# Performance work log

Hardware: AMD Instinct MI355X
Metric: run time of the kernel (lower is better)

## Reference

```python
import jax, jax.numpy as jnp
from jax import lax
import numpy as np

B, T, E, H, DA, HEADS, V = 128, 512, 256, 256, 25, 5, 2080
NEG = -1e30


def setup_inputs() -> dict:
    key = jax.random.key(0)
    ks = jax.random.split(key, 10)
    word_ids = jax.random.randint(ks[0], (B, T), 0, V)
    lengths = jax.random.randint(ks[1], (B,), 1, T + 1)  # >=1, original skips empty captions
    emb = jax.random.normal(ks[2], (V, E), dtype=jnp.float32)  # normal_(0,1) init
    sc = 0.05
    W_ih_f = jax.random.normal(ks[3], (4 * H, E), dtype=jnp.float32) * sc
    W_hh_f = jax.random.normal(ks[4], (4 * H, H), dtype=jnp.float32) * sc
    W_ih_b = jax.random.normal(ks[5], (4 * H, E), dtype=jnp.float32) * sc
    W_hh_b = jax.random.normal(ks[6], (4 * H, H), dtype=jnp.float32) * sc
    b_f = jnp.zeros((4 * H,), jnp.float32)  # biases init constant 0
    b_b = jnp.zeros((4 * H,), jnp.float32)
    W_s1 = jax.random.normal(ks[7], (DA, 2 * H), dtype=jnp.float32) * sc
    W_s2 = jax.random.normal(ks[8], (HEADS, DA), dtype=jnp.float32) * sc
    return dict(word_ids=word_ids, lengths=lengths, emb=emb,
                W_ih_f=W_ih_f, W_hh_f=W_hh_f, b_f=b_f,
                W_ih_b=W_ih_b, W_hh_b=W_hh_b, b_b=b_b,
                W_s1=W_s1, W_s2=W_s2)


def _lstm(x, W_ih, W_hh, b):
    # x: [B,T,E] -> outputs [B,T,H]; PyTorch gate order i,f,g,o; zero init state
    px = jnp.einsum('bte,ge->tbg', x, W_ih) + b  # [T,B,4H], input proj precomputed
    h0 = jnp.zeros((x.shape[0], W_hh.shape[1]), x.dtype)

    def step(carry, p):
        h, c = carry
        g = p + h @ W_hh.T
        i, f, gg, o = jnp.split(g, 4, axis=-1)
        c = jax.nn.sigmoid(f) * c + jax.nn.sigmoid(i) * jnp.tanh(gg)
        h = jax.nn.sigmoid(o) * jnp.tanh(c)
        return (h, c), h

    _, hs = lax.scan(step, (h0, h0), px)
    return hs.transpose(1, 0, 2)  # [B,T,H]


def _forward(word_ids, lengths, emb, W_ih_f, W_hh_f, b_f, W_ih_b, W_hh_b, b_b, W_s1, W_s2):
    x = emb[word_ids]  # [B,T,E]
    tpos = jnp.arange(T)
    mask = tpos[None, :] < lengths[:, None]  # [B,T] valid positions
    # per-sample reversal within its own length (garbage tail comes after valid prefix)
    rev_idx = jnp.clip(lengths[:, None] - 1 - tpos[None, :], 0)  # [B,T]
    x_rev = jnp.take_along_axis(x, rev_idx[:, :, None], axis=1)
    h_fwd = _lstm(x, W_ih_f, W_hh_f, b_f)                       # [B,T,H]
    h_bwd_rev = _lstm(x_rev, W_ih_b, W_hh_b, b_b)
    h_bwd = jnp.take_along_axis(h_bwd_rev, rev_idx[:, :, None], axis=1)  # back to original order
    Hc = jnp.concatenate([h_fwd, h_bwd], axis=-1)               # [B,T,2H]
    # attention: softmax over time per head, masked to valid length
    s = jnp.tanh(Hc @ W_s1.T) @ W_s2.T                          # [B,T,heads]
    logits = jnp.where(mask[:, :, None], s, NEG)
    A = jax.nn.softmax(logits, axis=1).transpose(0, 2, 1)       # [B,heads,T]
    A = A * mask[:, None, :].astype(A.dtype)                    # exact zeros outside length
    M = jnp.einsum('bht,btd->bhd', A, Hc)                       # [B,heads,2H]
    sentence_embeddings = M.reshape(M.shape[0], -1)             # [B, heads*2H]
    AAt = jnp.einsum('bht,bgt->bhg', A, A)
    AAt = AAt * (1.0 - jnp.eye(HEADS, dtype=AAt.dtype))         # zero diagonal
    penal = jnp.sum(AAt * AAt) / M.shape[0]                     # mean of Frobenius^2
    return sentence_embeddings, penal


def reference(word_ids, lengths, emb, W_ih_f, W_hh_f, b_f, W_ih_b, W_hh_b, b_b, W_s1, W_s2):
    return _forward(word_ids, lengths, emb, W_ih_f, W_hh_f, b_f, W_ih_b, W_hh_b, b_b, W_s1, W_s2)
```

## Files before the change

### kernel.cpp

```cpp
#include <hip/hip_runtime.h>
#include <math.h>

#define T 512
#define B 128
#define E 256
#define H 256
#define G 1024
#define DA 25
#define HEADS 5
#define V 2080
#define NEGINF (-1e30f)

static constexpr size_t WBT_OFF  = 0;
static constexpr size_t WIH_OFF  = 1048576;
static constexpr size_t WS1M_OFF = 2097152;
static constexpr size_t PX_OFF   = 2148352;
static constexpr size_t HC_OFF   = 69257216;
static constexpr size_t HBUF_OFF = 203474944;
static constexpr size_t CST_OFF  = 203737088;
static constexpr size_t A_OFF    = 203999232;
static constexpr size_t PART_OFF = 205309952;
static constexpr size_t EMBH_OFF = 205310464;
static constexpr size_t EMBH_END = EMBH_OFF + (size_t)V * E * 2;

static constexpr unsigned LSTM_LDS_BYTES = 160304;

typedef _Float16 half2v __attribute__((ext_vector_type(2)));
typedef _Float16 half8_ __attribute__((ext_vector_type(8)));
typedef float    f32x4  __attribute__((ext_vector_type(4)));

__device__ __forceinline__ float sigmoidf_(float x) { return 1.f / (1.f + expf(-x)); }

__device__ __forceinline__ unsigned short f2h_(float f) {
    _Float16 h = (_Float16)f;
    unsigned short u;
    __builtin_memcpy(&u, &h, 2);
    return u;
}

__device__ __forceinline__ float fdot2_(unsigned w, half2v h, float acc) {
#if __has_builtin(__builtin_amdgcn_fdot2)
    half2v wv;
    __builtin_memcpy(&wv, &w, 4);
    return __builtin_amdgcn_fdot2(wv, h, acc, false);
#else
    unsigned short lo = (unsigned short)(w & 0xffffu), hi = (unsigned short)(w >> 16);
    _Float16 w0, w1;
    __builtin_memcpy(&w0, &lo, 2);
    __builtin_memcpy(&w1, &hi, 2);
    return fmaf((float)w0, (float)h[0], fmaf((float)w1, (float)h[1], acc));
#endif
}

__device__ __forceinline__ half2v packh2_(float a, float b) {
    half2v h;
    h[0] = (_Float16)a;
    h[1] = (_Float16)b;
    return h;
}

__global__ __launch_bounds__(256) void prep_kernel(const float* __restrict__ Whf,
                                                   const float* __restrict__ Whb,
                                                   const float* __restrict__ Wif,
                                                   const float* __restrict__ Wib,
                                                   const float* __restrict__ Ws1,
                                                   const float* __restrict__ emb,
                                                   unsigned short* __restrict__ wbt,
                                                   unsigned short* __restrict__ wih,
                                                   unsigned short* __restrict__ ws1m,
                                                   unsigned short* __restrict__ embh) {
    int idx = blockIdx.x * 256 + threadIdx.x;
    if (idx < 2 * G * H) {
        int d = idx >> 18;
        int rem = idx & 262143;
        int r = rem >> 8;
        int k = rem & 255;
        const float* W = d ? Whb : Whf;
        int gate = r >> 8, j = r & 255;
        int k2 = k >> 1, ke = k & 1;
        wbt[(((size_t)d * 128 + k2) * 256 + j) * 8 + gate * 2 + ke] = f2h_(W[(size_t)r * H + k]);
        const float* Wi = d ? Wib : Wif;
        wih[((size_t)d * G + r) * 256 + k] = f2h_(Wi[(size_t)r * E + k]);
    }
    if (idx < 32 * 512) {
        int r = idx >> 9, k = idx & 511;
        ws1m[idx] = (r < DA) ? f2h_(Ws1[r * 512 + k]) : (unsigned short)0;
    }
    if (embh && idx < V * E) embh[idx] = f2h_(emb[idx]);
}

__global__ __launch_bounds__(256) void proj_kernel(const int* __restrict__ word_ids,
                                                   const int* __restrict__ lengths,
                                                   const float* __restrict__ emb,
                                                   const unsigned* __restrict__ embh,
                                                   const unsigned* __restrict__ wih,
                                                   const float* __restrict__ bf,
                                                   const float* __restrict__ bb,
                                                   float* __restrict__ pxc, int chunk) {
    int g0 = blockIdx.x * 64;
    int b  = blockIdx.y;
    int d  = blockIdx.z;
    int len = lengths[b];
    int t0 = chunk * 64;
    if (t0 >= len) return;
    const float* bias = d ? bb : bf;

    __shared__ _Float16 A_s[64][264];
    __shared__ _Float16 B_s[64][264];

    int tid = threadIdx.x;
    int sr = tid >> 2, sq = tid & 3;

    {
        int t = t0 + sr;
        int src = d ? max(len - 1 - t, 0) : t;
        int wid = word_ids[b * T + src];
        if (embh) {
            const uint4* ap = (const uint4*)embh + (size_t)wid * 32;
            #pragma unroll
            for (int c = 0; c < 8; c++) {
                uint4 v = ap[sq * 8 + c];
                *(uint4*)&A_s[sr][(sq * 8 + c) * 8] = v;
            }
        } else {
            const float4* ep = (const float4*)(emb + (size_t)wid * E);
            #pragma unroll
            for (int c = 0; c < 8; c++) {
                float4 x0 = ep[(sq * 8 + c) * 2];
                float4 x1 = ep[(sq * 8 + c) * 2 + 1];
                half8_ hv;
                hv[0] = (_Float16)x0.x; hv[1] = (_Float16)x0.y;
                hv[2] = (_Float16)x0.z; hv[3] = (_Float16)x0.w;
                hv[4] = (_Float16)x1.x; hv[5] = (_Float16)x1.y;
                hv[6] = (_Float16)x1.z; hv[7] = (_Float16)x1.w;
                *(half8_*)&A_s[sr][(sq * 8 + c) * 8] = hv;
            }
        }
        const uint4* bp = (const uint4*)wih + ((size_t)d * G + g0 + sr) * 32;
        #pragma unroll
        for (int c = 0; c < 8; c++) {
            uint4 v = bp[sq * 8 + c];
            *(uint4*)&B_s[sr][(sq * 8 + c) * 8] = v;
        }
    }
    __syncthreads();

    int lane = tid & 63, wave = tid >> 6;
    int m0 = (wave >> 1) * 32;
    int n0 = (wave & 1) * 32;
    int lr = lane & 15, lq = lane >> 4;

    f32x4 acc00 = {0.f, 0.f, 0.f, 0.f}, acc01 = {0.f, 0.f, 0.f, 0.f};
    f32x4 acc10 = {0.f, 0.f, 0.f, 0.f}, acc11 = {0.f, 0.f, 0.f, 0.f};

    #pragma unroll
    for (int k0 = 0; k0 < E; k0 += 32) {
        int ka = k0 + lq * 8;
        half8_ af0 = *(const half8_*)&A_s[m0 + lr][ka];
        half8_ af1 = *(const half8_*)&A_s[m0 + 16 + lr][ka];
        half8_ bf0 = *(const half8_*)&B_s[n0 + lr][ka];
        half8_ bf1 = *(const half8_*)&B_s[n0 + 16 + lr][ka];
        acc00 = __builtin_amdgcn_mfma_f32_16x16x32_f16(af0, bf0, acc00, 0, 0, 0);
        acc01 = __builtin_amdgcn_mfma_f32_16x16x32_f16(af0, bf1, acc01, 0, 0, 0);
        acc10 = __builtin_amdgcn_mfma_f32_16x16x32_f16(af1, bf0, acc10, 0, 0, 0);
        acc11 = __builtin_amdgcn_mfma_f32_16x16x32_f16(af1, bf1, acc11, 0, 0, 0);
    }

    float bia0 = bias[g0 + n0 + lr];
    float bia1 = bias[g0 + n0 + 16 + lr];
    #pragma unroll
    for (int mi = 0; mi < 2; mi++) {
        f32x4 ar0 = mi ? acc10 : acc00;
        f32x4 ar1 = mi ? acc11 : acc01;
        #pragma unroll
        for (int rr = 0; rr < 4; rr++) {
            int s = m0 + mi * 16 + lq * 4 + rr;
            float* dst = pxc + ((size_t)(d * 64 + s) * B + b) * G + g0;
            dst[n0 + lr]      = ar0[rr] + bia0;
            dst[n0 + 16 + lr] = ar1[rr] + bia1;
        }
    }
}

__global__ __launch_bounds__(1024) void lstm6_kernel(const int* __restrict__ lengths,
                                                     const unsigned* __restrict__ wbt,
                                                     const float* __restrict__ pxc,
                                                     float* __restrict__ hc_out,
                                                     float* __restrict__ hbuf,
                                                     float* __restrict__ cstate,
                                                     int chunk) {
    int b   = blockIdx.x;
    int d   = blockIdx.y;
    int tid = threadIdx.x;
    int j  = tid & 255;
    int kq = tid >> 8;

    int len = lengths[b];
    int t0 = chunk * 64;
    if (t0 >= len) return;
    int tend = min(t0 + 64, len);

    extern __shared__ char smem[];
    unsigned* hh   = (unsigned*)smem;
    float4*   part = (float4*)(smem + 512);
    uint4*    wst  = (uint4*)(smem + 12848);

    float* hbufg = hbuf + ((size_t)d * B + b) * 256;

    float c = 0.f, hreg = 0.f;
    if (chunk == 0) {
        if (tid < 128) hh[tid] = 0u;
    } else {
        if (kq == 0) c = cstate[((size_t)d * B + b) * H + j];
        if (tid < 128) {
            half2v hv2 = packh2_(hbufg[2 * tid], hbufg[2 * tid + 1]);
            unsigned hu;
            __builtin_memcpy(&hu, &hv2, 4);
            hh[tid] = hu;
        }
    }

    const uint4* wp  = (const uint4*)wbt + ((size_t)d * 128 + kq * 32) * 256 + j;
    const float* pxd = pxc + (size_t)d * 64 * B * G;

    #pragma unroll
    for (int r = 0; r < 9; r++)
        wst[(kq * 9 + r) * 256 + j] = wp[(size_t)r * 256];
    uint4 wr0  = wp[9 * 256],  wr1  = wp[10 * 256], wr2  = wp[11 * 256];
    uint4 wr3  = wp[12 * 256], wr4  = wp[13 * 256], wr5  = wp[14 * 256];
    uint4 wr6  = wp[15 * 256], wr7  = wp[16 * 256], wr8  = wp[17 * 256];
    uint4 wr9  = wp[18 * 256], wr10 = wp[19 * 256], wr11 = wp[20 * 256];
    uint4 wr12 = wp[21 * 256], wr13 = wp[22 * 256], wr14 = wp[23 * 256];
    __syncthreads();

    int hlane = kq * 32 + (tid & 31);

    for (int t = t0; t < tend; t++) {
        int s = t - t0;
        float p0, p1, p2, p3;
        if (kq == 0) {
            const float* pxs = pxd + ((size_t)s * B + b) * G;
            p0 = pxs[j];
            p1 = pxs[256 + j];
            p2 = pxs[512 + j];
            p3 = pxs[768 + j];
        }
        float a0 = 0.f, a1 = 0.f, a2 = 0.f, a3 = 0.f;

        unsigned hlv = hh[hlane];

        #define HROW(IDX) __builtin_amdgcn_readlane(hlv, IDX)

        #pragma unroll
        for (int r = 24; r < 32; r++) {
            uint4 wv = wp[(size_t)r * 256];
            unsigned hu = HROW(r);
            half2v hhv;
            __builtin_memcpy(&hhv, &hu, 4);
            a0 = fdot2_(wv.x, hhv, a0);
            a1 = fdot2_(wv.y, hhv, a1);
            a2 = fdot2_(wv.z, hhv, a2);
            a3 = fdot2_(wv.w, hhv, a3);
        }
        #pragma unroll
        for (int r = 0; r < 9; r++) {
            uint4 wv = wst[(kq * 9 + r) * 256 + j];
            unsigned hu = HROW(r);
            half2v hhv;
            __builtin_memcpy(&hhv, &hu, 4);
            a0 = fdot2_(wv.x, hhv, a0);
            a1 = fdot2_(wv.y, hhv, a1);
            a2 = fdot2_(wv.z, hhv, a2);
            a3 = fdot2_(wv.w, hhv, a3);
        }
        {
            unsigned hu;
            half2v hv;
            #define RES_DOT(WR, IDX)                                   \
                hu = HROW(IDX);                                        \
                __builtin_memcpy(&hv, &hu, 4);                         \
                a0 = fdot2_(WR.x, hv, a0); a1 = fdot2_(WR.y, hv, a1);  \
                a2 = fdot2_(WR.z, hv, a2); a3 = fdot2_(WR.w, hv, a3);
            RES_DOT(wr0, 9)
            RES_DOT(wr1, 10)
            RES_DOT(wr2, 11)
            RES_DOT(wr3, 12)
            RES_DOT(wr4, 13)
            RES_DOT(wr5, 14)
            RES_DOT(wr6, 15)
            RES_DOT(wr7, 16)
            RES_DOT(wr8, 17)
            RES_DOT(wr9, 18)
            RES_DOT(wr10, 19)
            RES_DOT(wr11, 20)
            RES_DOT(wr12, 21)
            RES_DOT(wr13, 22)
            RES_DOT(wr14, 23)
            #undef RES_DOT
        }
        #undef HROW

        if (kq > 0) part[(kq - 1) * 257 + j] = make_float4(a0, a1, a2, a3);
        __syncthreads();

        if (kq == 0) {
            #pragma unroll
            for (int q = 0; q < 3; q++) {
                float4 qv = part[q * 257 + j];
                a0 += qv.x; a1 += qv.y; a2 += qv.z; a3 += qv.w;
            }
            a0 += p0; a1 += p1; a2 += p2; a3 += p3;

            float ig = sigmoidf_(a0), fg = sigmoidf_(a1), og = sigmoidf_(a3);
            c = fg * c + ig * tanhf(a2);
            float h = og * tanhf(c);
            hreg = h;

            float hn = __shfl_down(h, 1);
            if (!(j & 1)) {
                half2v hv2 = packh2_(h, hn);
                unsigned hu;
                __builtin_memcpy(&hu, &hv2, 4);
                hh[j >> 1] = hu;
            }
            int pos = d ? (len - 1 - t) : t;
            hc_out[((size_t)b * T + pos) * (2 * H) + d * H + j] = h;
        }
        __syncthreads();
    }

    if (kq == 0) {
        cstate[((size_t)d * B + b) * H + j] = c;
        hbufg[j] = hreg;
    }
}

__global__ __launch_bounds__(256) void logits_kernel(const int* __restrict__ lengths,
                                                     const float* __restrict__ hc,
                                                     const uint4* __restrict__ ws1m,
                                                     const float* __restrict__ Ws2,
                                                     float* __restrict__ S) {
    __shared__ _Float16 A_s[64][520];
    __shared__ _Float16 B_s[32][520];

    int b = blockIdx.y, tt = blockIdx.x;
    int tid = threadIdx.x;
    int len = lengths[b];
    int t0 = tt * 64;

    int lane = tid & 63, wave = tid >> 6;
    int lr = lane & 15, lq = lane >> 4;
    int m0 = wave * 16;

    if (t0 >= len) {
        if (lr < HEADS) {
            #pragma unroll
            for (int rr = 0; rr < 4; rr++) {
                int t = t0 + m0 + lq * 4 + rr;
                S[((size_t)b * HEADS + lr) * T + t] = NEGINF;
            }
        }
        return;
    }

    {
        #pragma unroll
        for (int i = 0; i < 8; i++) {
            int u = tid + i * 256;
            int r = u >> 6, c8 = u & 63;
            *(uint4*)&B_s[r][c8 * 8] = ws1m[u];
        }
    }
    {
        int row = tid >> 2, q = tid & 3;
        int t = t0 + row;
        const float4* ep = (const float4*)(hc + ((size_t)b * T + t) * 512 + q * 128);
        #pragma unroll
        for (int c = 0; c < 16; c++) {
            float4 x0 = ep[2 * c];
            float4 x1 = ep[2 * c + 1];
            half8_ hv;
            hv[0] = (_Float16)x0.x; hv[1] = (_Float16)x0.y;
            hv[2] = (_Float16)x0.z; hv[3] = (_Float16)x0.w;
            hv[4] = (_Float16)x1.x; hv[5] = (_Float16)x1.y;
            hv[6] = (_Float16)x1.z; hv[7] = (_Float16)x1.w;
            *(half8_*)&A_s[row][q * 128 + c * 8] = hv;
        }
    }
    __syncthreads();

    f32x4 acc0 = {0.f, 0.f, 0.f, 0.f};
    f32x4 acc1 = {0.f, 0.f, 0.f, 0.f};
    #pragma unroll
    for (int ks = 0; ks < 16; ks++) {
        int ka = ks * 32 + lq * 8;
        half8_ af  = *(const half8_*)&A_s[m0 + lr][ka];
        half8_ bf0 = *(const half8_*)&B_s[lr][ka];
        half8_ bf1 = *(const half8_*)&B_s[16 + lr][ka];
        acc0 = __builtin_amdgcn_mfma_f32_16x16x32_f16(af, bf0, acc0, 0, 0, 0);
        acc1 = __builtin_amdgcn_mfma_f32_16x16x32_f16(af, bf1, acc1, 0, 0, 0);
    }

    float w2a[HEADS], w2b[HEADS];
    #pragma unroll
    for (int h = 0; h < HEADS; h++) {
        w2a[h] = Ws2[h * DA + lr];
        w2b[h] = (lr + 16 < DA) ? Ws2[h * DA + 16 + lr] : 0.f;
    }

    #pragma unroll
    for (int rr = 0; rr < 4; rr++) {
        float y0 = tanhf(acc0[rr]);
        float y1 = tanhf(acc1[rr]);
        int t = t0 + m0 + lq * 4 + rr;
        float sv[HEADS];
        #pragma unroll
        for (int h = 0; h < HEADS; h++) {
            float v = y0 * w2a[h] + y1 * w2b[h];
            v += __shfl_xor(v, 1, 16);
            v += __shfl_xor(v, 2, 16);
            v += __shfl_xor(v, 4, 16);
            v += __shfl_xor(v, 8, 16);
            sv[h] = v;
        }
        if (lr < HEADS) {
            S[((size_t)b * HEADS + lr) * T + t] = (t < len) ? sv[lr] : NEGINF;
        }
    }
}

__global__ __launch_bounds__(256) void softmax_kernel(float* __restrict__ S) {
    int row = blockIdx.x;
    float* p = S + (size_t)row * T;
    int tid = threadIdx.x;
    int lane = tid & 63, wave = tid >> 6;
    __shared__ float rr[4], ss[4];

    float mx = NEGINF;
    #pragma unroll
    for (int i = 0; i < 2; i++) mx = fmaxf(mx, p[tid + i * 256]);
    for (int off = 32; off; off >>= 1) mx = fmaxf(mx, __shfl_xor(mx, off, 64));
    if (lane == 0) rr[wave] = mx;
    __syncthreads();
    mx = fmaxf(fmaxf(rr[0], rr[1]), fmaxf(rr[2], rr[3]));

    float e[2], sum = 0.f;
    #pragma unroll
    for (int i = 0; i < 2; i++) { e[i] = expf(p[tid + i * 256] - mx); sum += e[i]; }
    for (int off = 32; off; off >>= 1) sum += __shfl_xor(sum, off, 64);
    if (lane == 0) ss[wave] = sum;
    __syncthreads();
    sum = ss[0] + ss[1] + ss[2] + ss[3];
    float inv = 1.f / sum;
    #pragma unroll
    for (int i = 0; i < 2; i++) p[tid + i * 256] = e[i] * inv;
}

__global__ __launch_bounds__(256) void attnM_kernel(const int* __restrict__ lengths,
                                                    const float* __restrict__ A,
                                                    const float* __restrict__ hc,
                                                    float* __restrict__ out,
                                                    float* __restrict__ part) {
    int b = blockIdx.x, tid = threadIdx.x;
    int len = lengths[b];
    const float* Ab  = A + (size_t)b * HEADS * T;
    const float* hcb = hc + (size_t)b * T * (2 * H);
    float acc[HEADS][2];
    #pragma unroll
    for (int h = 0; h < HEADS; h++) { acc[h][0] = 0.f; acc[h][1] = 0.f; }
    float p[10];
    #pragma unroll
    for (int i = 0; i < 10; i++) p[i] = 0.f;

    for (int t = 0; t < len; t++) {
        float v0 = hcb[(size_t)t * (2 * H) + tid];
        float v1 = hcb[(size_t)t * (2 * H) + H + tid];
        float a0 = Ab[t], a1 = Ab[T + t], a2 = Ab[2 * T + t], a3 = Ab[3 * T + t], a4 = Ab[4 * T + t];
        acc[0][0] += a0 * v0; acc[0][1] += a0 * v1;
        acc[1][0] += a1 * v0; acc[1][1] += a1 * v1;
        acc[2][0] += a2 * v0; acc[2][1] += a2 * v1;
        acc[3][0] += a3 * v0; acc[3][1] += a3 * v1;
        acc[4][0] += a4 * v0; acc[4][1] += a4 * v1;
        if ((t & 255) == tid) {
            p[0] += a0 * a1; p[1] += a0 * a2; p[2] += a0 * a3; p[3] += a0 * a4;
            p[4] += a1 * a2; p[5] += a1 * a3; p[6] += a1 * a4;
            p[7] += a2 * a3; p[8] += a2 * a4; p[9] += a3 * a4;
        }
    }
    #pragma unroll
    for (int h = 0; h < HEADS; h++) {
        out[(size_t)b * (HEADS * 2 * H) + h * (2 * H) + tid]     = acc[h][0];
        out[(size_t)b * (HEADS * 2 * H) + h * (2 * H) + H + tid] = acc[h][1];
    }

    __shared__ float red[10][4];
    int lane = tid & 63, wave = tid >> 6;
    #pragma unroll
    for (int i = 0; i < 10; i++) {
        float v = p[i];
        for (int off = 32; off; off >>= 1) v += __shfl_xor(v, off, 64);
        if (lane == 0) red[i][wave] = v;
    }
    __syncthreads();
    if (tid == 0) {
        float s = 0.f;
        #pragma unroll
        for (int i = 0; i < 10; i++) {
            float P = red[i][0] + red[i][1] + red[i][2] + red[i][3];
            s += 2.f * P * P;
        }
        part[b] = s;
    }
}

__global__ __launch_bounds__(128) void final_kernel(const float* __restrict__ part,
                                                    float* __restrict__ out) {
    int tid = threadIdx.x;
    float v = part[tid];
    for (int off = 32; off; off >>= 1) v += __shfl_xor(v, off, 64);
    __shared__ float r2[2];
    if ((tid & 63) == 0) r2[tid >> 6] = v;
    __syncthreads();
    if (tid == 0) out[(size_t)B * HEADS * 2 * H] = (r2[0] + r2[1]) * (1.f / (float)B);
}

extern "C" void kernel_launch(void* const* d_in, const int* in_sizes, int n_in,
                              void* d_out, int out_size, void* d_ws, size_t ws_size,
                              hipStream_t stream) {
    const int*   word_ids = (const int*)d_in[0];
    const int*   lengths  = (const int*)d_in[1];
    const float* emb      = (const float*)d_in[2];
    const float* W_ih_f   = (const float*)d_in[3];
    const float* W_hh_f   = (const float*)d_in[4];
    const float* b_f      = (const float*)d_in[5];
    const float* W_ih_b   = (const float*)d_in[6];
    const float* W_hh_b   = (const float*)d_in[7];
    const float* b_b      = (const float*)d_in[8];
    const float* W_s1     = (const float*)d_in[9];
    const float* W_s2     = (const float*)d_in[10];
    float* out = (float*)d_out;

    char* ws = (char*)d_ws;
    unsigned short* wbt16 = (unsigned short*)(ws + WBT_OFF);
    unsigned*       wbt   = (unsigned*)(ws + WBT_OFF);
    unsigned short* wih16 = (unsigned short*)(ws + WIH_OFF);
    unsigned*       wihu  = (unsigned*)(ws + WIH_OFF);
    unsigned short* ws1m16 = (unsigned short*)(ws + WS1M_OFF);
    const uint4*    ws1m4  = (const uint4*)(ws + WS1M_OFF);
    float* pxc    = (float*)(ws + PX_OFF);
    float* hc     = (float*)(ws + HC_OFF);
    float* hbuf   = (float*)(ws + HBUF_OFF);
    float* cstate = (float*)(ws + CST_OFF);
    float* Abuf   = (float*)(ws + A_OFF);
    float* part   = (float*)(ws + PART_OFF);
    bool have_embh = (ws_size >= EMBH_END);
    unsigned short* embh16 = have_embh ? (unsigned short*)(ws + EMBH_OFF) : nullptr;
    const unsigned* embhu  = have_embh ? (const unsigned*)(ws + EMBH_OFF) : nullptr;

    prep_kernel<<<2080, 256, 0, stream>>>(W_hh_f, W_hh_b, W_ih_f, W_ih_b, W_s1, emb,
                                          wbt16, wih16, ws1m16, embh16);

    for (int c = 0; c < 8; c++) {
        proj_kernel<<<dim3(16, 128, 2), 256, 0, stream>>>(
            word_ids, lengths, emb, embhu, wihu, b_f, b_b, pxc, c);
        lstm6_kernel<<<dim3(128, 2), 1024, LSTM_LDS_BYTES, stream>>>(
            lengths, wbt, pxc, hc, hbuf, cstate, c);
    }

    logits_kernel<<<dim3(8, 128), 256, 0, stream>>>(lengths, hc, ws1m4, W_s2, Abuf);
    softmax_kernel<<<B * HEADS, 256, 0, stream>>>(Abuf);
    attnM_kernel<<<B, 256, 0, stream>>>(lengths, Abuf, hc, out, part);
    final_kernel<<<1, 128, 0, stream>>>(part, out);
}
```

Baseline: 1.497 ms.

## Speed up LSTM recurrence step with fast gate math and deferred output stores

In the recurrent LSTM kernel, the sigmoid and tanh gates now use hardware exp2/rcp approximations instead of expf and tanhf. The global store of each h value is deferred to the start of the next step so it does not sit on the critical path. Global weight loads are hoisted so they overlap with the dot products. The shuffle-and-pack h write is replaced by direct 16-bit LDS stores, and the gate phase runs at raised wave priority with a min-blocks launch bound. The approximate transcendentals may change accuracy slightly, and the launch bound can shift register allocation.

```diff
diff --git a/kernel.cpp b/kernel.cpp
--- a/kernel.cpp
+++ b/kernel.cpp
@@ -29,7 +29,25 @@
 typedef _Float16 half8_ __attribute__((ext_vector_type(8)));
 typedef float    f32x4  __attribute__((ext_vector_type(4)));
 
+#if __has_builtin(__builtin_amdgcn_exp2f)
+#define EXP2F_(x) __builtin_amdgcn_exp2f(x)
+#else
+#define EXP2F_(x) exp2f(x)
+#endif
+#if __has_builtin(__builtin_amdgcn_rcpf)
+#define RCPF_(x) __builtin_amdgcn_rcpf(x)
+#else
+#define RCPF_(x) (1.0f / (x))
+#endif
+
 __device__ __forceinline__ float sigmoidf_(float x) { return 1.f / (1.f + expf(-x)); }
+
+__device__ __forceinline__ float sigmoid_fast_(float x) {
+    return RCPF_(1.f + EXP2F_(-1.44269504f * x));
+}
+__device__ __forceinline__ float tanh_fast_(float x) {
+    return 1.f - 2.f * RCPF_(1.f + EXP2F_(2.88539008f * x));
+}
 
 __device__ __forceinline__ unsigned short f2h_(float f) {
     _Float16 h = (_Float16)f;
@@ -182,13 +200,13 @@
     }
 }
 
-__global__ __launch_bounds__(1024) void lstm6_kernel(const int* __restrict__ lengths,
-                                                     const unsigned* __restrict__ wbt,
-                                                     const float* __restrict__ pxc,
-                                                     float* __restrict__ hc_out,
-                                                     float* __restrict__ hbuf,
-                                                     float* __restrict__ cstate,
-                                                     int chunk) {
+__global__ __launch_bounds__(1024, 4) void lstm6_kernel(const int* __restrict__ lengths,
+                                                        const unsigned* __restrict__ wbt,
+                                                        const float* __restrict__ pxc,
+                                                        float* __restrict__ hc_out,
+                                                        float* __restrict__ hbuf,
+                                                        float* __restrict__ cstate,
+                                                        int chunk) {
     int b   = blockIdx.x;
     int d   = blockIdx.y;
     int tid = threadIdx.x;
@@ -204,6 +222,7 @@
     unsigned* hh   = (unsigned*)smem;
     float4*   part = (float4*)(smem + 512);
     uint4*    wst  = (uint4*)(smem + 12848);
+    unsigned short* hh16 = (unsigned short*)smem;
 
     float* hbufg = hbuf + ((size_t)d * B + b) * 256;
 
@@ -234,9 +253,14 @@
     __syncthreads();
 
     int hlane = kq * 32 + (tid & 31);
+    int pendpos = -1;
 
     for (int t = t0; t < tend; t++) {
         int s = t - t0;
+
+        if (kq == 0 && pendpos >= 0)
+            hc_out[((size_t)b * T + pendpos) * (2 * H) + d * H + j] = hreg;
+
         float p0, p1, p2, p3;
         if (kq == 0) {
             const float* pxs = pxd + ((size_t)s * B + b) * G;
@@ -245,65 +269,39 @@
             p2 = pxs[512 + j];
             p3 = pxs[768 + j];
         }
+
+        unsigned hlv = hh[hlane];
+        uint4 wv0 = wp[24 * 256], wv1 = wp[25 * 256], wv2 = wp[26 * 256], wv3 = wp[27 * 256];
+
         float a0 = 0.f, a1 = 0.f, a2 = 0.f, a3 = 0.f;
 
-        unsigned hlv = hh[hlane];
-
         #define HROW(IDX) __builtin_amdgcn_readlane(hlv, IDX)
-
-        #pragma unroll
-        for (int r = 24; r < 32; r++) {
-            uint4 wv = wp[(size_t)r * 256];
-            unsigned hu = HROW(r);
-            half2v hhv;
-            __builtin_memcpy(&hhv, &hu, 4);
-            a0 = fdot2_(wv.x, hhv, a0);
-            a1 = fdot2_(wv.y, hhv, a1);
-            a2 = fdot2_(wv.z, hhv, a2);
-            a3 = fdot2_(wv.w, hhv, a3);
-        }
+        #define DOT4(WV, IDX)                                          \
+            { unsigned hu = HROW(IDX); half2v hx;                      \
+              __builtin_memcpy(&hx, &hu, 4);                           \
+              a0 = fdot2_(WV.x, hx, a0); a1 = fdot2_(WV.y, hx, a1);    \
+              a2 = fdot2_(WV.z, hx, a2); a3 = fdot2_(WV.w, hx, a3); }
+
         #pragma unroll
         for (int r = 0; r < 9; r++) {
             uint4 wv = wst[(kq * 9 + r) * 256 + j];
-            unsigned hu = HROW(r);
-            half2v hhv;
-            __builtin_memcpy(&hhv, &hu, 4);
-            a0 = fdot2_(wv.x, hhv, a0);
-            a1 = fdot2_(wv.y, hhv, a1);
-            a2 = fdot2_(wv.z, hhv, a2);
-            a3 = fdot2_(wv.w, hhv, a3);
-        }
-        {
-            unsigned hu;
-            half2v hv;
-            #define RES_DOT(WR, IDX)                                   \
-                hu = HROW(IDX);                                        \
-                __builtin_memcpy(&hv, &hu, 4);                         \
-                a0 = fdot2_(WR.x, hv, a0); a1 = fdot2_(WR.y, hv, a1);  \
-                a2 = fdot2_(WR.z, hv, a2); a3 = fdot2_(WR.w, hv, a3);
-            RES_DOT(wr0, 9)
-            RES_DOT(wr1, 10)
-            RES_DOT(wr2, 11)
-            RES_DOT(wr3, 12)
-            RES_DOT(wr4, 13)
-            RES_DOT(wr5, 14)
-            RES_DOT(wr6, 15)
-            RES_DOT(wr7, 16)
-            RES_DOT(wr8, 17)
-            RES_DOT(wr9, 18)
-            RES_DOT(wr10, 19)
-            RES_DOT(wr11, 20)
-            RES_DOT(wr12, 21)
-            RES_DOT(wr13, 22)
-            RES_DOT(wr14, 23)
-            #undef RES_DOT
-        }
+            DOT4(wv, r)
+        }
+        DOT4(wv0, 24) DOT4(wv1, 25) DOT4(wv2, 26) DOT4(wv3, 27)
+        uint4 wv4 = wp[28 * 256], wv5 = wp[29 * 256], wv6 = wp[30 * 256], wv7 = wp[31 * 256];
+        DOT4(wr0, 9)  DOT4(wr1, 10)  DOT4(wr2, 11)  DOT4(wr3, 12)
+        DOT4(wr4, 13) DOT4(wr5, 14)  DOT4(wr6, 15)  DOT4(wr7, 16)
+        DOT4(wr8, 17) DOT4(wr9, 18)  DOT4(wr10, 19) DOT4(wr11, 20)
+        DOT4(wr12, 21) DOT4(wr13, 22) DOT4(wr14, 23)
+        DOT4(wv4, 28) DOT4(wv5, 29) DOT4(wv6, 30) DOT4(wv7, 31)
+        #undef DOT4
         #undef HROW
 
         if (kq > 0) part[(kq - 1) * 257 + j] = make_float4(a0, a1, a2, a3);
         __syncthreads();
 
         if (kq == 0) {
+            __builtin_amdgcn_s_setprio(1);
             #pragma unroll
             for (int q = 0; q < 3; q++) {
                 float4 qv = part[q * 257 + j];
@@ -311,25 +309,20 @@
             }
             a0 += p0; a1 += p1; a2 += p2; a3 += p3;
 
-            float ig = sigmoidf_(a0), fg = sigmoidf_(a1), og = sigmoidf_(a3);
-            c = fg * c + ig * tanhf(a2);
-            float h = og * tanhf(c);
+            float ig = sigmoid_fast_(a0), fg = sigmoid_fast_(a1), og = sigmoid_fast_(a3);
+            c = fg * c + ig * tanh_fast_(a2);
+            float h = og * tanh_fast_(c);
             hreg = h;
-
-            float hn = __shfl_down(h, 1);
-            if (!(j & 1)) {
-                half2v hv2 = packh2_(h, hn);
-                unsigned hu;
-                __builtin_memcpy(&hu, &hv2, 4);
-                hh[j >> 1] = hu;
-            }
-            int pos = d ? (len - 1 - t) : t;
-            hc_out[((size_t)b * T + pos) * (2 * H) + d * H + j] = h;
+            hh16[j] = f2h_(h);
+            pendpos = d ? (len - 1 - t) : t;
+            __builtin_amdgcn_s_setprio(0);
         }
         __syncthreads();
     }
 
     if (kq == 0) {
+        if (pendpos >= 0)
+            hc_out[((size_t)b * T + pendpos) * (2 * H) + d * H + j] = hreg;
         cstate[((size_t)d * B + b) * H + j] = c;
         hbufg[j] = hreg;
     }
```

Measured after the change: 1.303 ms. 12.9% less time.
